# Kernel tuning notes

Measured on AMD Instinct MI355X. Metric: run time of the kernel, lower is better.

Reference implementation:

```python
import math
import jax, jax.numpy as jnp
import numpy as np

B, L, D, H = 2, 2048, 1024, 16
DH = D // H

def setup_inputs() -> dict:
    key = jax.random.key(0)
    ks = jax.random.split(key, 8)
    def xavier(k, fan_in, fan_out, shape):
        lim = math.sqrt(6.0 / (fan_in + fan_out))
        return jax.random.uniform(k, shape, jnp.float32, -lim, lim)
    x = jax.random.normal(ks[0], (B, L, D), jnp.float32)
    mask = jnp.ones((B, L), jnp.int32)
    # weights stored (in, out) so y = x @ W + b (equivalent to torch Linear)
    W_qkv = xavier(ks[1], D, 3 * D, (D, 3 * D))
    b_qkv = jnp.zeros((3 * D,), jnp.float32)
    W_out = xavier(ks[2], D, D, (D, D))
    b_out = jnp.zeros((D,), jnp.float32)
    W_phase = xavier(ks[3], D, H, (D, H))
    b_phase = jax.random.normal(ks[4], (H,), jnp.float32) * 0.02
    resonance_scale = jnp.float32(0.1)
    phase_scale = jnp.float32(1.0)
    return {"x": x, "mask": mask, "W_qkv": W_qkv, "b_qkv": b_qkv,
            "W_out": W_out, "b_out": b_out, "W_phase": W_phase,
            "b_phase": b_phase, "resonance_scale": resonance_scale,
            "phase_scale": phase_scale}

def reference(x, mask, W_qkv, b_qkv, W_out, b_out, W_phase, b_phase,
              resonance_scale, phase_scale):
    # qkv: (B,L,3D) -> (3,B,H,L,dh)
    qkv = (x @ W_qkv + b_qkv).reshape(B, L, 3, H, DH).transpose(2, 0, 3, 1, 4)
    q, k, v = qkv[0], qkv[1], qkv[2]
    scores = jnp.einsum('bhqd,bhkd->bhqk', q, k) / math.sqrt(DH)
    # per-token per-head phase (B,H,L)
    phase_val = jnp.tanh(phase_scale * (x @ W_phase + b_phase)).transpose(0, 2, 1)
    phase_diff = (phase_val[:, :, :, None] - phase_val[:, :, None, :]) ** 2
    scores = scores - resonance_scale * phase_diff
    # mask: (B,L) -> (B,1,1,L)
    m = mask[:, None, None, :]
    scores = jnp.where(m == 0, jnp.float32(-1e9), scores)
    attn = jax.nn.softmax(scores, axis=-1)
    out = jnp.einsum('bhqk,bhkd->bhqd', attn, v)  # (B,H,L,dh)
    out = out.transpose(0, 2, 1, 3).reshape(B, L, D)
    return out @ W_out + b_out
```

## Files before the change

### kernel.cpp

```cpp
#include <hip/hip_runtime.h>

typedef unsigned short u16;
typedef unsigned int u32;
typedef __attribute__((ext_vector_type(2))) unsigned long long u64x2;
typedef __attribute__((ext_vector_type(4))) unsigned short u16x4;
typedef __attribute__((ext_vector_type(8))) __bf16 bf16x8;
typedef __attribute__((ext_vector_type(4))) float f32x4;
typedef __attribute__((ext_vector_type(2))) float f32x2;

#define DEV static __device__ __forceinline__
#define LOG2E 1.4426950408889634f

DEV u16 f2bf(float f) { __bf16 h = (__bf16)f; return __builtin_bit_cast(u16, h); }

#define BB   2
#define LLEN 2048
#define DDIM 1024
#define HH   16
#define DH   64
#define MTOT 4096
#define N3   3072

DEV void gl16(const void* g, void* l) {
  __builtin_amdgcn_global_load_lds(
      (const __attribute__((address_space(1))) void*)g,
      (__attribute__((address_space(3))) void*)l, 16, 0, 0);
}
DEV void gl4(const void* g, void* l) {
  __builtin_amdgcn_global_load_lds(
      (const __attribute__((address_space(1))) void*)g,
      (__attribute__((address_space(3))) void*)l, 4, 0, 0);
}

DEV void stage64(const u16* org, size_t gsb, u16* lds, int lane, int wid) {
#pragma unroll
  for (int j = 0; j < 2; j++) {
    int inst = wid * 2 + j;
    int r8 = lane >> 3;
    int row = inst * 8 + r8;
    int s = (r8 & 3) | ((inst & 1) << 2);
    const char* src = (const char*)org + (size_t)row * gsb +
                      (((lane & 7) ^ s) << 4);
    gl16(src, (char*)lds + inst * 1024);
  }
}
DEV bf16x8 read128s(const u16* tile, int row, int colb) {
  return *reinterpret_cast<const bf16x8*>(
      (const char*)tile + row * 128 +
      (colb ^ (((row & 3) | (((row >> 3) & 1) << 2)) << 4)));
}

DEV void stage128x32(const u16* org, size_t gsb, u16* lds, int lane, int wid) {
#pragma unroll
  for (int j = 0; j < 2; j++) {
    int inst = wid + j * 4;
    int r16 = lane >> 2;
    const char* src = (const char*)org + (size_t)(inst * 16 + r16) * gsb +
                      ((((lane & 3) ^ (r16 & 3))) << 4);
    gl16(src, (char*)lds + inst * 1024);
  }
}
DEV bf16x8 read64(const u16* tile, int row, int colb) {
  return *reinterpret_cast<const bf16x8*>(
      (const char*)tile + row * 64 + (colb ^ ((row & 3) << 4)));
}

__global__ __launch_bounds__(256) void k_cvt(const float* __restrict__ in,
                                             u16* __restrict__ out, int n) {
  int i = (blockIdx.x * 256 + threadIdx.x) * 4;
  if (i < n) {
    f32x4 v = *reinterpret_cast<const f32x4*>(in + i);
    u16x4 o;
    o.x = f2bf(v.x); o.y = f2bf(v.y); o.z = f2bf(v.z); o.w = f2bf(v.w);
    *reinterpret_cast<u16x4*>(out + i) = o;
  }
}

__global__ __launch_bounds__(256) void k_transpose_w(const float* __restrict__ W,
                                                     u16* __restrict__ WT,
                                                     int K, int N) {
  __shared__ float s[32][33];
  int k0 = blockIdx.x * 32, n0 = blockIdx.y * 32;
  int tx = threadIdx.x & 31, ty = threadIdx.x >> 5;
#pragma unroll
  for (int i = 0; i < 4; i++)
    s[ty + i * 8][tx] = W[(k0 + ty + i * 8) * (size_t)N + n0 + tx];
  __syncthreads();
#pragma unroll
  for (int i = 0; i < 4; i++)
    WT[(size_t)(n0 + ty + i * 8) * K + k0 + tx] = f2bf(s[tx][ty + i * 8]);
}

__global__ __launch_bounds__(256) void k_phase(const float* __restrict__ x,
                                               const float* __restrict__ Wp,
                                               const float* __restrict__ bp,
                                               const float* __restrict__ pscale,
                                               const float* __restrict__ rscale,
                                               const int* __restrict__ mask,
                                               f32x2* __restrict__ ppk) {
  int m = blockIdx.x;
  int t = threadIdx.x;
  int h = t & 15, j = t >> 4;
  const float* xr = x + (size_t)m * DDIM;
  float acc = 0.f;
#pragma unroll 4
  for (int kk = 0; kk < 64; kk++) {
    int k = j * 64 + kk;
    acc += xr[k] * Wp[k * HH + h];
  }
  __shared__ float s[16][17];
  s[j][h] = acc;
  __syncthreads();
  if (t < 16) {
    float sum = 0.f;
#pragma unroll
    for (int jj = 0; jj < 16; jj++) sum += s[jj][t];
    float v = tanhf((*pscale) * (sum + bp[t]));
    int b = m >> 11, l = m & (LLEN - 1);
    float kb = (mask[m] == 0) ? -1.0e9f : (-(*rscale) * LOG2E) * v * v;
    f32x2 o; o.x = v; o.y = kb;
    ppk[((size_t)(b * HH + t)) * LLEN + l] = o;
  }
}

template <bool BF16_OUT>
__global__ __launch_bounds__(256) void k_gemm(const u16* __restrict__ A,
                                              const u16* __restrict__ BT,
                                              const float* __restrict__ bias,
                                              void* __restrict__ C,
                                              int M, int N, int K) {
  __shared__ __attribute__((aligned(16))) u16 sA[2][128 * 32];
  __shared__ __attribute__((aligned(16))) u16 sB[2][128 * 32];
  int m0 = blockIdx.x * 128, n0 = blockIdx.y * 128;
  int t = threadIdx.x, lane = t & 63, wid = t >> 6;
  int wm = wid >> 1, wn = wid & 1;
  int lc = lane & 15, lg = lane >> 4;

  const u16* Ao = A + (size_t)m0 * K;
  const u16* Bo = BT + (size_t)n0 * K;

  f32x4 acc[4][4] = {};
  stage128x32(Ao, (size_t)K * 2, sA[0], lane, wid);
  stage128x32(Bo, (size_t)K * 2, sB[0], lane, wid);
  __syncthreads();
  int cur = 0;
  int NT = K >> 5;
  for (int kt = 0; kt < NT; kt++) {
    if (kt + 1 < NT) {
      stage128x32(Ao + (kt + 1) * 32, (size_t)K * 2, sA[cur ^ 1], lane, wid);
      stage128x32(Bo + (kt + 1) * 32, (size_t)K * 2, sB[cur ^ 1], lane, wid);
    }
    bf16x8 af[4], bfr[4];
#pragma unroll
    for (int i = 0; i < 4; i++) af[i] = read64(sA[cur], wm * 64 + i * 16 + lc, lg * 16);
#pragma unroll
    for (int j = 0; j < 4; j++) bfr[j] = read64(sB[cur], wn * 64 + j * 16 + lc, lg * 16);
    __builtin_amdgcn_s_setprio(1);
#pragma unroll
    for (int i = 0; i < 4; i++)
#pragma unroll
      for (int j = 0; j < 4; j++)
        acc[i][j] = __builtin_amdgcn_mfma_f32_16x16x32_bf16(af[i], bfr[j], acc[i][j], 0, 0, 0);
    __builtin_amdgcn_s_setprio(0);
    __syncthreads();
    cur ^= 1;
  }

  int rg = lane >> 4;
#pragma unroll
  for (int i = 0; i < 4; i++) {
#pragma unroll
    for (int j = 0; j < 4; j++) {
      int col = n0 + wn * 64 + j * 16 + lc;
      float bv = bias[col];
#pragma unroll
      for (int r = 0; r < 4; r++) {
        int row = m0 + wm * 64 + i * 16 + rg * 4 + r;
        float v = acc[i][j][r] + bv;
        if (BF16_OUT)
          ((u16*)C)[(size_t)row * N + col] = f2bf(v);
        else
          ((float*)C)[(size_t)row * N + col] = v;
      }
    }
  }
}

__global__ __launch_bounds__(256) void k_vtrans(const u16* __restrict__ qkv,
                                                u16* __restrict__ vT) {
  int bh = blockIdx.y;
  int lt = blockIdx.x;
  int b = bh >> 4, h = bh & 15;
  __shared__ __attribute__((aligned(16))) u16 s[64][72];
  int t = threadIdx.x;
#pragma unroll
  for (int i = 0; i < 2; i++) {
    int c = t + i * 256;
    int l = c >> 3, ko = (c & 7) * 8;
    *reinterpret_cast<u64x2*>(&s[l][ko]) = *reinterpret_cast<const u64x2*>(
        &qkv[(size_t)(b * LLEN + lt * 64 + l) * N3 + 2 * DDIM + h * DH + ko]);
  }
  __syncthreads();
#pragma unroll
  for (int i = 0; i < 2; i++) {
    int c = t + i * 256;
    int dh = c >> 3, lo = (c & 7) * 8;
    u16 tmp[8];
#pragma unroll
    for (int j = 0; j < 8; j++) tmp[j] = s[lo + j][dh];
    *reinterpret_cast<u64x2*>(&vT[((size_t)bh * DH + dh) * LLEN + lt * 64 + lo]) =
        *reinterpret_cast<u64x2*>(tmp);
  }
}

__global__ __launch_bounds__(256, 4) void k_attn(const u16* __restrict__ qkv,
                                                 const u16* __restrict__ vT,
                                                 const f32x2* __restrict__ ppk,
                                                 const float* __restrict__ rscale_p,
                                                 u16* __restrict__ attn_out) {
  __shared__ __attribute__((aligned(16))) u16 kS[2][64 * 64];
  __shared__ __attribute__((aligned(16))) u16 vS[2][64 * 64];
  __shared__ __attribute__((aligned(16))) float ppS[2][128];

  int bh = blockIdx.y, b = bh >> 4, h = bh & 15;
  int q0 = blockIdx.x * 64;
  int t = threadIdx.x, lane = t & 63, wid = t >> 6;
  int qb = q0 + wid * 16;
  int lc = lane & 15, lg = lane >> 4;

  const float rs2 = (*rscale_p) * LOG2E;
  const float c1 = 0.125f * LOG2E;
  const f32x2* pprow = ppk + (size_t)bh * LLEN;
  const float* pprowf = (const float*)pprow;

  bf16x8 qf0, qf1;
  {
    const u16* qp = &qkv[(size_t)(b * LLEN + qb + lc) * N3 + h * DH + lg * 8];
    qf0 = *reinterpret_cast<const bf16x8*>(qp);
    qf1 = *reinterpret_cast<const bf16x8*>(qp + 32);
  }
  float wq = 2.f * rs2 * pprow[qb + lc].x;

  const u16* kg = qkv + (size_t)(b * LLEN) * N3 + DDIM + h * DH;
  const u16* vg = vT + (size_t)bh * DH * LLEN;

  stage64(kg, (size_t)N3 * 2, kS[0], lane, wid);
  stage64(vg, (size_t)LLEN * 2, vS[0], lane, wid);
  gl4(pprowf + lane, &ppS[0][0]);
  gl4(pprowf + 64 + lane, &ppS[0][64]);

  f32x4 o[4] = {};
  float mrow = -1e30f, lrow = 0.f;
  int arow = ((lc >> 2) << 3) | (lc & 3);

  int cur = 0;
  const int NT = LLEN / 64;
  for (int kt = 0; kt < NT; kt++) {
    int kb = kt * 64;
    if (kt + 1 < NT) {
      stage64(kg + (size_t)(kb + 64) * N3, (size_t)N3 * 2, kS[cur ^ 1], lane, wid);
      stage64(vg + kb + 64, (size_t)LLEN * 2, vS[cur ^ 1], lane, wid);
      const float* pt = pprowf + (size_t)(kb + 64) * 2;
      gl4(pt + lane, &ppS[cur ^ 1][0]);
      gl4(pt + 64 + lane, &ppS[cur ^ 1][64]);
      asm volatile("s_waitcnt vmcnt(6)" ::: "memory");
    } else {
      asm volatile("s_waitcnt vmcnt(0)" ::: "memory");
    }
    __builtin_amdgcn_s_barrier();

    f32x4 sv[4];
#pragma unroll
    for (int blk = 0; blk < 4; blk++) {
      int krow = arow + ((blk & 2) << 4) + ((blk & 1) << 2);
      bf16x8 kf0 = read128s(kS[cur], krow, lg * 16);
      bf16x8 kf1 = read128s(kS[cur], krow, 64 + lg * 16);
      f32x4 z = {};
      __builtin_amdgcn_s_setprio(1);
      z = __builtin_amdgcn_mfma_f32_16x16x32_bf16(kf0, qf0, z, 0, 0, 0);
      z = __builtin_amdgcn_mfma_f32_16x16x32_bf16(kf1, qf1, z, 0, 0, 0);
      __builtin_amdgcn_s_setprio(0);
      sv[blk] = z;
    }

    {
      const float* pt = &ppS[cur][0];
#pragma unroll
      for (int blk = 0; blk < 4; blk++) {
        int off2 = (((blk & 2) << 4) + ((blk & 1) << 2) + lg * 8) * 2;
        f32x4 p0 = *reinterpret_cast<const f32x4*>(pt + off2);
        f32x4 p1 = *reinterpret_cast<const f32x4*>(pt + off2 + 4);
        sv[blk][0] = fmaf(sv[blk][0], c1, fmaf(wq, p0.x, p0.y));
        sv[blk][1] = fmaf(sv[blk][1], c1, fmaf(wq, p0.z, p0.w));
        sv[blk][2] = fmaf(sv[blk][2], c1, fmaf(wq, p1.x, p1.y));
        sv[blk][3] = fmaf(sv[blk][3], c1, fmaf(wq, p1.z, p1.w));
      }
    }

    float rm = sv[0][0];
#pragma unroll
    for (int blk = 0; blk < 4; blk++)
#pragma unroll
      for (int r = 0; r < 4; r++) rm = fmaxf(rm, sv[blk][r]);
    rm = fmaxf(rm, __shfl_xor(rm, 16, 64));
    rm = fmaxf(rm, __shfl_xor(rm, 32, 64));

    if (!__all(rm <= mrow + 8.f)) {
      float mn = fmaxf(mrow, rm);
      float al = __builtin_amdgcn_exp2f(mrow - mn);
      mrow = mn;
      lrow *= al;
      float ao0 = __shfl(al, lg * 4 + 0, 16);
      float ao1 = __shfl(al, lg * 4 + 1, 16);
      float ao2 = __shfl(al, lg * 4 + 2, 16);
      float ao3 = __shfl(al, lg * 4 + 3, 16);
#pragma unroll
      for (int d = 0; d < 4; d++) {
        o[d][0] *= ao0; o[d][1] *= ao1; o[d][2] *= ao2; o[d][3] *= ao3;
      }
    }

    float ssum = 0.f;
#pragma unroll
    for (int blk = 0; blk < 4; blk++)
#pragma unroll
      for (int r = 0; r < 4; r++) {
        float p = __builtin_amdgcn_exp2f(sv[blk][r] - mrow);
        sv[blk][r] = p;
        ssum += p;
      }
    ssum += __shfl_xor(ssum, 16, 64);
    ssum += __shfl_xor(ssum, 32, 64);
    lrow += ssum;

    bf16x8 pa0, pa1;
#pragma unroll
    for (int r = 0; r < 4; r++) {
      pa0[r] = (__bf16)sv[0][r];
      pa0[4 + r] = (__bf16)sv[1][r];
      pa1[r] = (__bf16)sv[2][r];
      pa1[4 + r] = (__bf16)sv[3][r];
    }

#pragma unroll
    for (int d = 0; d < 4; d++) {
      bf16x8 vb0 = read128s(vS[cur], d * 16 + lc, lg * 16);
      bf16x8 vb1 = read128s(vS[cur], d * 16 + lc, 64 + lg * 16);
      __builtin_amdgcn_s_setprio(1);
      o[d] = __builtin_amdgcn_mfma_f32_16x16x32_bf16(pa0, vb0, o[d], 0, 0, 0);
      o[d] = __builtin_amdgcn_mfma_f32_16x16x32_bf16(pa1, vb1, o[d], 0, 0, 0);
      __builtin_amdgcn_s_setprio(0);
    }

    __builtin_amdgcn_s_barrier();
    cur ^= 1;
  }

  float linv = 1.0f / lrow;
  float li0 = __shfl(linv, lg * 4 + 0, 16);
  float li1 = __shfl(linv, lg * 4 + 1, 16);
  float li2 = __shfl(linv, lg * 4 + 2, 16);
  float li3 = __shfl(linv, lg * 4 + 3, 16);
#pragma unroll
  for (int d = 0; d < 4; d++) {
    int col = h * DH + d * 16 + lc;
    size_t base = (size_t)(b * LLEN + qb + lg * 4) * DDIM + col;
    attn_out[base] = f2bf(o[d][0] * li0);
    attn_out[base + DDIM] = f2bf(o[d][1] * li1);
    attn_out[base + 2 * DDIM] = f2bf(o[d][2] * li2);
    attn_out[base + 3 * DDIM] = f2bf(o[d][3] * li3);
  }
}

extern "C" void kernel_launch(void* const* d_in, const int* in_sizes, int n_in,
                              void* d_out, int out_size, void* d_ws, size_t ws_size,
                              hipStream_t stream) {
  const float* x       = (const float*)d_in[0];
  const int*   mask    = (const int*)d_in[1];
  const float* W_qkv   = (const float*)d_in[2];
  const float* b_qkv   = (const float*)d_in[3];
  const float* W_out   = (const float*)d_in[4];
  const float* b_out   = (const float*)d_in[5];
  const float* W_phase = (const float*)d_in[6];
  const float* b_phase = (const float*)d_in[7];
  const float* rscale  = (const float*)d_in[8];
  const float* pscale  = (const float*)d_in[9];
  float* out = (float*)d_out;

  char* ws = (char*)d_ws;
  u16* x_bf     = (u16*)(ws + 0);
  u16* wt_qkv   = (u16*)(ws + 8388608);
  u16* wt_out   = (u16*)(ws + 14680064);
  u16* qkv      = (u16*)(ws + 16777216);
  u16* vT       = (u16*)(ws + 41943040);
  u16* attn_out = (u16*)(ws + 50331648);
  f32x2* ppk    = (f32x2*)(ws + 58720256);

  k_cvt<<<MTOT * DDIM / 4 / 256, 256, 0, stream>>>(x, x_bf, MTOT * DDIM);
  k_transpose_w<<<dim3(DDIM / 32, N3 / 32), 256, 0, stream>>>(W_qkv, wt_qkv, DDIM, N3);
  k_transpose_w<<<dim3(DDIM / 32, DDIM / 32), 256, 0, stream>>>(W_out, wt_out, DDIM, DDIM);
  k_phase<<<MTOT, 256, 0, stream>>>(x, W_phase, b_phase, pscale, rscale, mask, ppk);
  k_gemm<true><<<dim3(MTOT / 128, N3 / 128), 256, 0, stream>>>(
      x_bf, wt_qkv, b_qkv, qkv, MTOT, N3, DDIM);
  k_vtrans<<<dim3(LLEN / 64, BB * HH), 256, 0, stream>>>(qkv, vT);
  k_attn<<<dim3(LLEN / 64, BB * HH), 256, 0, stream>>>(
      qkv, vT, ppk, rscale, attn_out);
  k_gemm<false><<<dim3(MTOT / 128, DDIM / 128), 256, 0, stream>>>(
      attn_out, wt_out, b_out, out, MTOT, DDIM, DDIM);
}
```

Baseline: 234.9 us.

## Fuse x conversion into phase kernel, V transpose into QKV GEMM, remap attention blocks

The standalone fp32-to-bf16 conversion kernel is removed and the phase kernel now writes bf16 x while it reads x with vector loads. The QKV GEMM writes the V slice directly in transposed layout, so the separate V transpose kernel and its reread of qkv are gone. The attention kernel remaps block indices so all query tiles of a head land on the same XCD for L2 reuse of K/V, and its key loop is unrolled by two with fixed buffer indices. The costs are extra launches removed against narrower 8-byte strided stores for V and a larger unrolled attention body that may raise register pressure.

```diff
diff --git a/kernel.cpp b/kernel.cpp
--- a/kernel.cpp
+++ b/kernel.cpp
@@ -2,6 +2,7 @@
 
 typedef unsigned short u16;
 typedef unsigned int u32;
+typedef unsigned long long u64;
 typedef __attribute__((ext_vector_type(2))) unsigned long long u64x2;
 typedef __attribute__((ext_vector_type(4))) unsigned short u16x4;
 typedef __attribute__((ext_vector_type(8))) __bf16 bf16x8;
@@ -65,17 +66,6 @@
       (const char*)tile + row * 64 + (colb ^ ((row & 3) << 4)));
 }
 
-__global__ __launch_bounds__(256) void k_cvt(const float* __restrict__ in,
-                                             u16* __restrict__ out, int n) {
-  int i = (blockIdx.x * 256 + threadIdx.x) * 4;
-  if (i < n) {
-    f32x4 v = *reinterpret_cast<const f32x4*>(in + i);
-    u16x4 o;
-    o.x = f2bf(v.x); o.y = f2bf(v.y); o.z = f2bf(v.z); o.w = f2bf(v.w);
-    *reinterpret_cast<u16x4*>(out + i) = o;
-  }
-}
-
 __global__ __launch_bounds__(256) void k_transpose_w(const float* __restrict__ W,
                                                      u16* __restrict__ WT,
                                                      int K, int N) {
@@ -97,16 +87,28 @@
                                                const float* __restrict__ pscale,
                                                const float* __restrict__ rscale,
                                                const int* __restrict__ mask,
-                                               f32x2* __restrict__ ppk) {
+                                               f32x2* __restrict__ ppk,
+                                               u16* __restrict__ x_bf) {
   int m = blockIdx.x;
   int t = threadIdx.x;
   int h = t & 15, j = t >> 4;
   const float* xr = x + (size_t)m * DDIM;
+  u16* xbr = x_bf + (size_t)m * DDIM;
+  const float* wpb = Wp + h;
   float acc = 0.f;
 #pragma unroll 4
-  for (int kk = 0; kk < 64; kk++) {
-    int k = j * 64 + kk;
-    acc += xr[k] * Wp[k * HH + h];
+  for (int kk4 = 0; kk4 < 16; kk4++) {
+    int k0 = j * 64 + kk4 * 4;
+    f32x4 xv = *reinterpret_cast<const f32x4*>(xr + k0);
+    acc = fmaf(xv.x, wpb[(k0 + 0) * HH], acc);
+    acc = fmaf(xv.y, wpb[(k0 + 1) * HH], acc);
+    acc = fmaf(xv.z, wpb[(k0 + 2) * HH], acc);
+    acc = fmaf(xv.w, wpb[(k0 + 3) * HH], acc);
+    if (h == 0) {
+      u16x4 o;
+      o.x = f2bf(xv.x); o.y = f2bf(xv.y); o.z = f2bf(xv.z); o.w = f2bf(xv.w);
+      *reinterpret_cast<u16x4*>(xbr + k0) = o;
+    }
   }
   __shared__ float s[16][17];
   s[j][h] = acc;
@@ -123,11 +125,12 @@
   }
 }
 
-template <bool BF16_OUT>
+template <bool BF16_OUT, bool QKV>
 __global__ __launch_bounds__(256) void k_gemm(const u16* __restrict__ A,
                                               const u16* __restrict__ BT,
                                               const float* __restrict__ bias,
                                               void* __restrict__ C,
+                                              u16* __restrict__ vT,
                                               int M, int N, int K) {
   __shared__ __attribute__((aligned(16))) u16 sA[2][128 * 32];
   __shared__ __attribute__((aligned(16))) u16 sB[2][128 * 32];
@@ -167,6 +170,24 @@
   }
 
   int rg = lane >> 4;
+  if (QKV && n0 >= 2 * DDIM) {
+#pragma unroll
+    for (int i = 0; i < 4; i++) {
+      int rowb = m0 + wm * 64 + i * 16 + rg * 4;
+      int bb = rowb >> 11, l = rowb & (LLEN - 1);
+#pragma unroll
+      for (int j = 0; j < 4; j++) {
+        int vcol = n0 - 2 * DDIM + wn * 64 + j * 16 + lc;
+        float bv = bias[n0 + wn * 64 + j * 16 + lc];
+        u16 tmp[4];
+#pragma unroll
+        for (int r = 0; r < 4; r++) tmp[r] = f2bf(acc[i][j][r] + bv);
+        *reinterpret_cast<u64*>(&vT[(size_t)vcol * LLEN + bb * (HH * DH * LLEN) + l]) =
+            *reinterpret_cast<u64*>(tmp);
+      }
+    }
+    return;
+  }
 #pragma unroll
   for (int i = 0; i < 4; i++) {
 #pragma unroll
@@ -186,33 +207,6 @@
   }
 }
 
-__global__ __launch_bounds__(256) void k_vtrans(const u16* __restrict__ qkv,
-                                                u16* __restrict__ vT) {
-  int bh = blockIdx.y;
-  int lt = blockIdx.x;
-  int b = bh >> 4, h = bh & 15;
-  __shared__ __attribute__((aligned(16))) u16 s[64][72];
-  int t = threadIdx.x;
-#pragma unroll
-  for (int i = 0; i < 2; i++) {
-    int c = t + i * 256;
-    int l = c >> 3, ko = (c & 7) * 8;
-    *reinterpret_cast<u64x2*>(&s[l][ko]) = *reinterpret_cast<const u64x2*>(
-        &qkv[(size_t)(b * LLEN + lt * 64 + l) * N3 + 2 * DDIM + h * DH + ko]);
-  }
-  __syncthreads();
-#pragma unroll
-  for (int i = 0; i < 2; i++) {
-    int c = t + i * 256;
-    int dh = c >> 3, lo = (c & 7) * 8;
-    u16 tmp[8];
-#pragma unroll
-    for (int j = 0; j < 8; j++) tmp[j] = s[lo + j][dh];
-    *reinterpret_cast<u64x2*>(&vT[((size_t)bh * DH + dh) * LLEN + lt * 64 + lo]) =
-        *reinterpret_cast<u64x2*>(tmp);
-  }
-}
-
 __global__ __launch_bounds__(256, 4) void k_attn(const u16* __restrict__ qkv,
                                                  const u16* __restrict__ vT,
                                                  const f32x2* __restrict__ ppk,
@@ -222,8 +216,11 @@
   __shared__ __attribute__((aligned(16))) u16 vS[2][64 * 64];
   __shared__ __attribute__((aligned(16))) float ppS[2][128];
 
-  int bh = blockIdx.y, b = bh >> 4, h = bh & 15;
-  int q0 = blockIdx.x * 64;
+  int lin = blockIdx.y * 32 + blockIdx.x;
+  int xcd = lin & 7, slot = lin >> 3;
+  int bh = xcd * 4 + (slot >> 5);
+  int q0 = (slot & 31) * 64;
+  int b = bh >> 4, h = bh & 15;
   int t = threadIdx.x, lane = t & 63, wid = t >> 6;
   int qb = q0 + wid * 16;
   int lc = lane & 15, lg = lane >> 4;
@@ -253,108 +250,96 @@
   float mrow = -1e30f, lrow = 0.f;
   int arow = ((lc >> 2) << 3) | (lc & 3);
 
-  int cur = 0;
-  const int NT = LLEN / 64;
-  for (int kt = 0; kt < NT; kt++) {
-    int kb = kt * 64;
-    if (kt + 1 < NT) {
-      stage64(kg + (size_t)(kb + 64) * N3, (size_t)N3 * 2, kS[cur ^ 1], lane, wid);
-      stage64(vg + kb + 64, (size_t)LLEN * 2, vS[cur ^ 1], lane, wid);
-      const float* pt = pprowf + (size_t)(kb + 64) * 2;
-      gl4(pt + lane, &ppS[cur ^ 1][0]);
-      gl4(pt + 64 + lane, &ppS[cur ^ 1][64]);
-      asm volatile("s_waitcnt vmcnt(6)" ::: "memory");
-    } else {
-      asm volatile("s_waitcnt vmcnt(0)" ::: "memory");
-    }
-    __builtin_amdgcn_s_barrier();
-
-    f32x4 sv[4];
-#pragma unroll
-    for (int blk = 0; blk < 4; blk++) {
-      int krow = arow + ((blk & 2) << 4) + ((blk & 1) << 2);
-      bf16x8 kf0 = read128s(kS[cur], krow, lg * 16);
-      bf16x8 kf1 = read128s(kS[cur], krow, 64 + lg * 16);
-      f32x4 z = {};
-      __builtin_amdgcn_s_setprio(1);
-      z = __builtin_amdgcn_mfma_f32_16x16x32_bf16(kf0, qf0, z, 0, 0, 0);
-      z = __builtin_amdgcn_mfma_f32_16x16x32_bf16(kf1, qf1, z, 0, 0, 0);
-      __builtin_amdgcn_s_setprio(0);
-      sv[blk] = z;
-    }
-
-    {
-      const float* pt = &ppS[cur][0];
-#pragma unroll
-      for (int blk = 0; blk < 4; blk++) {
-        int off2 = (((blk & 2) << 4) + ((blk & 1) << 2) + lg * 8) * 2;
-        f32x4 p0 = *reinterpret_cast<const f32x4*>(pt + off2);
-        f32x4 p1 = *reinterpret_cast<const f32x4*>(pt + off2 + 4);
-        sv[blk][0] = fmaf(sv[blk][0], c1, fmaf(wq, p0.x, p0.y));
-        sv[blk][1] = fmaf(sv[blk][1], c1, fmaf(wq, p0.z, p0.w));
-        sv[blk][2] = fmaf(sv[blk][2], c1, fmaf(wq, p1.x, p1.y));
-        sv[blk][3] = fmaf(sv[blk][3], c1, fmaf(wq, p1.z, p1.w));
-      }
-    }
-
-    float rm = sv[0][0];
-#pragma unroll
-    for (int blk = 0; blk < 4; blk++)
-#pragma unroll
-      for (int r = 0; r < 4; r++) rm = fmaxf(rm, sv[blk][r]);
-    rm = fmaxf(rm, __shfl_xor(rm, 16, 64));
-    rm = fmaxf(rm, __shfl_xor(rm, 32, 64));
-
-    if (!__all(rm <= mrow + 8.f)) {
-      float mn = fmaxf(mrow, rm);
-      float al = __builtin_amdgcn_exp2f(mrow - mn);
-      mrow = mn;
-      lrow *= al;
-      float ao0 = __shfl(al, lg * 4 + 0, 16);
-      float ao1 = __shfl(al, lg * 4 + 1, 16);
-      float ao2 = __shfl(al, lg * 4 + 2, 16);
-      float ao3 = __shfl(al, lg * 4 + 3, 16);
-#pragma unroll
-      for (int d = 0; d < 4; d++) {
-        o[d][0] *= ao0; o[d][1] *= ao1; o[d][2] *= ao2; o[d][3] *= ao3;
-      }
-    }
-
-    float ssum = 0.f;
-#pragma unroll
-    for (int blk = 0; blk < 4; blk++)
-#pragma unroll
-      for (int r = 0; r < 4; r++) {
-        float p = __builtin_amdgcn_exp2f(sv[blk][r] - mrow);
-        sv[blk][r] = p;
-        ssum += p;
-      }
-    ssum += __shfl_xor(ssum, 16, 64);
-    ssum += __shfl_xor(ssum, 32, 64);
-    lrow += ssum;
-
-    bf16x8 pa0, pa1;
-#pragma unroll
-    for (int r = 0; r < 4; r++) {
-      pa0[r] = (__bf16)sv[0][r];
-      pa0[4 + r] = (__bf16)sv[1][r];
-      pa1[r] = (__bf16)sv[2][r];
-      pa1[4 + r] = (__bf16)sv[3][r];
-    }
-
-#pragma unroll
-    for (int d = 0; d < 4; d++) {
-      bf16x8 vb0 = read128s(vS[cur], d * 16 + lc, lg * 16);
-      bf16x8 vb1 = read128s(vS[cur], d * 16 + lc, 64 + lg * 16);
-      __builtin_amdgcn_s_setprio(1);
-      o[d] = __builtin_amdgcn_mfma_f32_16x16x32_bf16(pa0, vb0, o[d], 0, 0, 0);
-      o[d] = __builtin_amdgcn_mfma_f32_16x16x32_bf16(pa1, vb1, o[d], 0, 0, 0);
-      __builtin_amdgcn_s_setprio(0);
-    }
-
-    __builtin_amdgcn_s_barrier();
-    cur ^= 1;
-  }
+#define ATTN_STEP(KB, CUR)                                                     \
+  do {                                                                         \
+    if ((KB) + 64 < LLEN) {                                                    \
+      stage64(kg + (size_t)((KB) + 64) * N3, (size_t)N3 * 2, kS[(CUR) ^ 1],    \
+              lane, wid);                                                      \
+      stage64(vg + (KB) + 64, (size_t)LLEN * 2, vS[(CUR) ^ 1], lane, wid);     \
+      const float* pt_ = pprowf + (size_t)((KB) + 64) * 2;                     \
+      gl4(pt_ + lane, &ppS[(CUR) ^ 1][0]);                                     \
+      gl4(pt_ + 64 + lane, &ppS[(CUR) ^ 1][64]);                               \
+      asm volatile("s_waitcnt vmcnt(6)" ::: "memory");                         \
+    } else {                                                                   \
+      asm volatile("s_waitcnt vmcnt(0)" ::: "memory");                         \
+    }                                                                          \
+    __builtin_amdgcn_s_barrier();                                              \
+    f32x4 sv[4];                                                               \
+    _Pragma("unroll") for (int blk = 0; blk < 4; blk++) {                      \
+      int krow = arow + ((blk & 2) << 4) + ((blk & 1) << 2);                   \
+      bf16x8 kf0 = read128s(kS[CUR], krow, lg * 16);                           \
+      bf16x8 kf1 = read128s(kS[CUR], krow, 64 + lg * 16);                      \
+      f32x4 z = {};                                                            \
+      __builtin_amdgcn_s_setprio(1);                                           \
+      z = __builtin_amdgcn_mfma_f32_16x16x32_bf16(kf0, qf0, z, 0, 0, 0);       \
+      z = __builtin_amdgcn_mfma_f32_16x16x32_bf16(kf1, qf1, z, 0, 0, 0);       \
+      __builtin_amdgcn_s_setprio(0);                                           \
+      sv[blk] = z;                                                             \
+    }                                                                          \
+    {                                                                          \
+      const float* pt_ = &ppS[CUR][0];                                         \
+      _Pragma("unroll") for (int blk = 0; blk < 4; blk++) {                    \
+        int off2 = (((blk & 2) << 4) + ((blk & 1) << 2) + lg * 8) * 2;         \
+        f32x4 p0 = *reinterpret_cast<const f32x4*>(pt_ + off2);                \
+        f32x4 p1 = *reinterpret_cast<const f32x4*>(pt_ + off2 + 4);            \
+        sv[blk][0] = fmaf(sv[blk][0], c1, fmaf(wq, p0.x, p0.y));               \
+        sv[blk][1] = fmaf(sv[blk][1], c1, fmaf(wq, p0.z, p0.w));               \
+        sv[blk][2] = fmaf(sv[blk][2], c1, fmaf(wq, p1.x, p1.y));               \
+        sv[blk][3] = fmaf(sv[blk][3], c1, fmaf(wq, p1.z, p1.w));               \
+      }                                                                        \
+    }                                                                          \
+    float rm = sv[0][0];                                                       \
+    _Pragma("unroll") for (int blk = 0; blk < 4; blk++)                        \
+        _Pragma("unroll") for (int r = 0; r < 4; r++)                          \
+            rm = fmaxf(rm, sv[blk][r]);                                        \
+    rm = fmaxf(rm, __shfl_xor(rm, 16, 64));                                    \
+    rm = fmaxf(rm, __shfl_xor(rm, 32, 64));                                    \
+    if (!__all(rm <= mrow + 8.f)) {                                            \
+      float mn = fmaxf(mrow, rm);                                              \
+      float al = __builtin_amdgcn_exp2f(mrow - mn);                            \
+      mrow = mn;                                                               \
+      lrow *= al;                                                              \
+      float ao0 = __shfl(al, lg * 4 + 0, 16);                                  \
+      float ao1 = __shfl(al, lg * 4 + 1, 16);                                  \
+      float ao2 = __shfl(al, lg * 4 + 2, 16);                                  \
+      float ao3 = __shfl(al, lg * 4 + 3, 16);                                  \
+      _Pragma("unroll") for (int d = 0; d < 4; d++) {                          \
+        o[d][0] *= ao0; o[d][1] *= ao1; o[d][2] *= ao2; o[d][3] *= ao3;        \
+      }                                                                        \
+    }                                                                          \
+    float ssum = 0.f;                                                          \
+    _Pragma("unroll") for (int blk = 0; blk < 4; blk++)                        \
+        _Pragma("unroll") for (int r = 0; r < 4; r++) {                        \
+      float p = __builtin_amdgcn_exp2f(sv[blk][r] - mrow);                     \
+      sv[blk][r] = p;                                                          \
+      ssum += p;                                                               \
+    }                                                                          \
+    ssum += __shfl_xor(ssum, 16, 64);                                          \
+    ssum += __shfl_xor(ssum, 32, 64);                                          \
+    lrow += ssum;                                                              \
+    bf16x8 pa0, pa1;                                                           \
+    _Pragma("unroll") for (int r = 0; r < 4; r++) {                            \
+      pa0[r] = (__bf16)sv[0][r];                                               \
+      pa0[4 + r] = (__bf16)sv[1][r];                                           \
+      pa1[r] = (__bf16)sv[2][r];                                               \
+      pa1[4 + r] = (__bf16)sv[3][r];                                           \
+    }                                                                          \
+    _Pragma("unroll") for (int d = 0; d < 4; d++) {                            \
+      bf16x8 vb0 = read128s(vS[CUR], d * 16 + lc, lg * 16);                    \
+      bf16x8 vb1 = read128s(vS[CUR], d * 16 + lc, 64 + lg * 16);               \
+      __builtin_amdgcn_s_setprio(1);                                           \
+      o[d] = __builtin_amdgcn_mfma_f32_16x16x32_bf16(pa0, vb0, o[d], 0, 0, 0); \
+      o[d] = __builtin_amdgcn_mfma_f32_16x16x32_bf16(pa1, vb1, o[d], 0, 0, 0); \
+      __builtin_amdgcn_s_setprio(0);                                           \
+    }                                                                          \
+    __builtin_amdgcn_s_barrier();                                              \
+  } while (0)
+
+  for (int kt = 0; kt < LLEN / 64; kt += 2) {
+    ATTN_STEP(kt * 64, 0);
+    ATTN_STEP(kt * 64 + 64, 1);
+  }
+#undef ATTN_STEP
 
   float linv = 1.0f / lrow;
   float li0 = __shfl(linv, lg * 4 + 0, 16);
@@ -396,15 +381,13 @@
   u16* attn_out = (u16*)(ws + 50331648);
   f32x2* ppk    = (f32x2*)(ws + 58720256);
 
-  k_cvt<<<MTOT * DDIM / 4 / 256, 256, 0, stream>>>(x, x_bf, MTOT * DDIM);
   k_transpose_w<<<dim3(DDIM / 32, N3 / 32), 256, 0, stream>>>(W_qkv, wt_qkv, DDIM, N3);
   k_transpose_w<<<dim3(DDIM / 32, DDIM / 32), 256, 0, stream>>>(W_out, wt_out, DDIM, DDIM);
-  k_phase<<<MTOT, 256, 0, stream>>>(x, W_phase, b_phase, pscale, rscale, mask, ppk);
-  k_gemm<true><<<dim3(MTOT / 128, N3 / 128), 256, 0, stream>>>(
-      x_bf, wt_qkv, b_qkv, qkv, MTOT, N3, DDIM);
-  k_vtrans<<<dim3(LLEN / 64, BB * HH), 256, 0, stream>>>(qkv, vT);
+  k_phase<<<MTOT, 256, 0, stream>>>(x, W_phase, b_phase, pscale, rscale, mask, ppk, x_bf);
+  k_gemm<true, true><<<dim3(MTOT / 128, N3 / 128), 256, 0, stream>>>(
+      x_bf, wt_qkv, b_qkv, qkv, vT, MTOT, N3, DDIM);
   k_attn<<<dim3(LLEN / 64, BB * HH), 256, 0, stream>>>(
       qkv, vT, ppk, rscale, attn_out);
-  k_gemm<false><<<dim3(MTOT / 128, DDIM / 128), 256, 0, stream>>>(
-      attn_out, wt_out, b_out, out, MTOT, DDIM, DDIM);
-}
+  k_gemm<false, false><<<dim3(MTOT / 128, DDIM / 128), 256, 0, stream>>>(
+      attn_out, wt_out, b_out, out, nullptr, MTOT, DDIM, DDIM);
+}
```

New measurement: 249.0 us. +6.0%, slower.
